# Kernel tuning notes

Measured on AMD Instinct MI355X. Metric: run time of the kernel, lower is better.

## Reference

```python
import jax, jax.numpy as jnp
import numpy as np

EMBED_DIM = 1024
NUM_HEADS = 16
HEAD_DIM = EMBED_DIM // NUM_HEADS


def setup_inputs() -> dict:
    key = jax.random.key(0)
    ks = jax.random.split(key, 9)
    B, S, E = 2, 2048, EMBED_DIM
    scale = 1.0 / np.sqrt(E)
    inputs = jax.random.normal(ks[0], (B, S, E), dtype=jnp.float32)
    # torch nn.Linear params: weight [out,in], bias [out]
    Wq = jax.random.uniform(ks[1], (E, E), jnp.float32, -scale, scale)
    bq = jax.random.uniform(ks[2], (E,), jnp.float32, -scale, scale)
    Wk = jax.random.uniform(ks[3], (E, E), jnp.float32, -scale, scale)
    bk = jax.random.uniform(ks[4], (E,), jnp.float32, -scale, scale)
    Wv = jax.random.uniform(ks[5], (E, E), jnp.float32, -scale, scale)
    bv = jax.random.uniform(ks[6], (E,), jnp.float32, -scale, scale)
    Wo = jax.random.uniform(ks[7], (E, E), jnp.float32, -scale, scale)
    bo = jax.random.uniform(ks[8], (E,), jnp.float32, -scale, scale)
    return {"inputs": inputs, "Wq": Wq, "bq": bq, "Wk": Wk, "bk": bk,
            "Wv": Wv, "bv": bv, "Wo": Wo, "bo": bo}


def _split_heads(x, B, S):
    # [B,S,E] -> [B,H,S,Dh]
    return x.reshape(B, S, NUM_HEADS, HEAD_DIM).transpose(0, 2, 1, 3)


def reference(inputs, Wq, bq, Wk, bk, Wv, bv, Wo, bo):
    B, S, E = inputs.shape
    q = _split_heads(inputs @ Wq.T + bq, B, S)
    k = _split_heads(inputs @ Wk.T + bk, B, S)
    v = _split_heads(inputs @ Wv.T + bv, B, S)
    inv_sqrt_dk = 1.0 / jnp.sqrt(jnp.float32(HEAD_DIM))
    scores = jnp.einsum('bhqd,bhkd->bhqk', q, k) * inv_sqrt_dk
    weights = jax.nn.softmax(scores, axis=-1)
    attn = jnp.einsum('bhqk,bhkd->bhqd', weights, v)
    concat = attn.transpose(0, 2, 1, 3).reshape(B, S, E)
    return concat @ Wo.T + bo
```

## Files before the change

### kernel.cpp

```cpp
#include <hip/hip_runtime.h>
#include <hip/hip_bf16.h>
#include <stdint.h>


typedef short bf16x8 __attribute__((ext_vector_type(8)));
typedef float f32x4 __attribute__((ext_vector_type(4)));

__device__ __forceinline__ unsigned short f2b(float x) {
    unsigned b = __float_as_uint(x);
    b += 0x7FFFu + ((b >> 16) & 1u);
    return (unsigned short)(b >> 16);
}
__device__ __forceinline__ float b2f(unsigned short u) {
    return __uint_as_float(((unsigned)u) << 16);
}
__device__ __forceinline__ f32x4 mfma16(bf16x8 a, bf16x8 b, f32x4 c) {
    return __builtin_amdgcn_mfma_f32_16x16x32_bf16(a, b, c, 0, 0, 0);
}
__device__ __forceinline__ void gl16(const void* g, void* l) {
    __builtin_amdgcn_global_load_lds(
        (const __attribute__((address_space(1))) void*)g,
        (__attribute__((address_space(3))) void*)l, 16, 0, 0);
}

__global__ __launch_bounds__(256)
void round4_kernel(const float* __restrict__ X, const float* __restrict__ Wq,
                   const float* __restrict__ Wk, const float* __restrict__ Wv,
                   unsigned short* __restrict__ Xh, unsigned short* __restrict__ Wh) {
    int i = blockIdx.x * 256 + threadIdx.x;
    const float4* src;
    ushort4* dst;
    if (i < 1048576) {
        src = (const float4*)X + i;
        dst = (ushort4*)Xh + i;
    } else {
        const int j = i - 1048576;
        const int w = j >> 18;
        const int k = j & 262143;
        const float* S = (w == 0) ? Wq : (w == 1) ? Wk : Wv;
        src = (const float4*)S + k;
        dst = (ushort4*)Wh + j;
    }
    float4 v = *src;
    ushort4 h;
    h.x = f2b(v.x); h.y = f2b(v.y); h.z = f2b(v.z); h.w = f2b(v.w);
    *dst = h;
}

__global__ void split_kernel(const float* __restrict__ src,
                             unsigned short* __restrict__ hi,
                             unsigned short* __restrict__ lo, int n4) {
    int i = blockIdx.x * blockDim.x + threadIdx.x;
    if (i >= n4) return;
    float4 v = reinterpret_cast<const float4*>(src)[i];
    ushort4 h, l;
    h.x = f2b(v.x); l.x = f2b(v.x - b2f(h.x));
    h.y = f2b(v.y); l.y = f2b(v.y - b2f(h.y));
    h.z = f2b(v.z); l.z = f2b(v.z - b2f(h.z));
    h.w = f2b(v.w); l.w = f2b(v.w - b2f(h.w));
    reinterpret_cast<ushort4*>(hi)[i] = h;
    reinterpret_cast<ushort4*>(lo)[i] = l;
}

__global__ __launch_bounds__(256, 2)
void gemm_qkv(const unsigned short* __restrict__ Xh, const unsigned short* __restrict__ Wh,
              const float* __restrict__ bias,
              unsigned short* __restrict__ Qs,
              unsigned short* __restrict__ Kh,
              unsigned short* __restrict__ Vh) {
    __shared__ __align__(16) unsigned short sA[128][32];
    __shared__ __align__(16) unsigned short sB[128][32];

    const int tid = threadIdx.x;
    const int lane = tid & 63;
    const int wid = tid >> 6;
    const int wr = wid >> 1, wc = wid & 1;
    const int m0 = blockIdx.y * 128, n0 = blockIdx.x * 128;
    const int fr = lane & 15;
    const int fo = (lane >> 4) << 3;
    const int rgrp = lane >> 4;
    constexpr float SC = 0.18033688011112042f;

    f32x4 zero4 = {0.f, 0.f, 0.f, 0.f};
    f32x4 acc[4][4];
#pragma unroll
    for (int i = 0; i < 4; i++)
#pragma unroll
        for (int j = 0; j < 4; j++) acc[i][j] = zero4;

    for (int k0 = 0; k0 < 1024; k0 += 32) {
        __syncthreads();
#pragma unroll
        for (int q = 0; q < 2; q++) {
            const int u = q * 256 + tid;
            const int row = u >> 2, c = u & 3;
            gl16(Xh + (size_t)(m0 + row) * 1024 + k0 + c * 8, (char*)&sA[0][0] + u * 16);
            gl16(Wh + (size_t)(n0 + row) * 1024 + k0 + c * 8, (char*)&sB[0][0] + u * 16);
        }
        __syncthreads();

        bf16x8 aF[4], bF[4];
#pragma unroll
        for (int i = 0; i < 4; i++) {
            aF[i] = *(const bf16x8*)&sA[wr * 64 + i * 16 + fr][fo];
            bF[i] = *(const bf16x8*)&sB[wc * 64 + i * 16 + fr][fo];
        }
#pragma unroll
        for (int i = 0; i < 4; i++)
#pragma unroll
            for (int j = 0; j < 4; j++)
                acc[i][j] = mfma16(aF[i], bF[j], acc[i][j]);
    }

#pragma unroll
    for (int i = 0; i < 4; i++) {
#pragma unroll
        for (int j = 0; j < 4; j++) {
            const int col = n0 + wc * 64 + j * 16 + fr;
            const float bv = bias[col];
            const int which = col >> 10;
            const int nn = col & 1023;
            const int h = nn >> 6, d = nn & 63;
#pragma unroll
            for (int r = 0; r < 4; r++) {
                const int row = m0 + wr * 64 + i * 16 + rgrp * 4 + r;
                const float v = acc[i][j][r] + bv;
                const int b = row >> 11, s = row & 2047;
                const size_t o = (((size_t)(b * 16 + h)) * 2048 + s) * 64 + d;
                if (which == 0)      Qs[o] = f2b(v * SC);
                else if (which == 1) Kh[o] = f2b(v);
                else                 Vh[o] = f2b(v);
            }
        }
    }
}

__global__ __launch_bounds__(256)
void vtrans(const unsigned short* __restrict__ V, unsigned short* __restrict__ Vt) {
    __shared__ unsigned short L[64][72];
    const int t = threadIdx.x;
    const int bh = blockIdx.y, s0 = blockIdx.x * 64;
    const size_t ib = (size_t)bh * 2048 * 64;
    const int srow = t >> 2, sc = (t & 3) * 16;
    *(uint4*)&L[srow][sc]     = *(const uint4*)(V + ib + (size_t)(s0 + srow) * 64 + sc);
    *(uint4*)&L[srow][sc + 8] = *(const uint4*)(V + ib + (size_t)(s0 + srow) * 64 + sc + 8);
    __syncthreads();
    const int d = t >> 2, k0 = (t & 3) * 16;
    unsigned short tmp[16];
#pragma unroll
    for (int i = 0; i < 16; i++) tmp[i] = L[k0 + i][d];
    *(uint4*)(Vt + ib + (size_t)d * 2048 + s0 + k0)     = *(uint4*)&tmp[0];
    *(uint4*)(Vt + ib + (size_t)d * 2048 + s0 + k0 + 8) = *(uint4*)&tmp[8];
}

__global__ __launch_bounds__(512)
void attn_kernel(const unsigned short* __restrict__ Qs,
                 const unsigned short* __restrict__ Kh,
                 const unsigned short* __restrict__ Vt,
                 unsigned short* __restrict__ OutHi, unsigned short* __restrict__ OutLo) {
    __shared__ __align__(16) unsigned short sK[2][64][64];
    __shared__ __align__(16) unsigned short sV[2][64][64];

    const int tid = threadIdx.x, lane = tid & 63, wid = tid >> 6;
    const int bh = blockIdx.y;
    const int q0 = blockIdx.x * 128;
    const int fr = lane & 15, fo = (lane >> 4) << 3, rgrp = lane >> 4;
    const size_t baseQK = (size_t)bh * 2048 * 64;
    const size_t baseVt = (size_t)bh * 64 * 2048;

    const int srow = tid >> 3, sc = tid & 7;
    const int klofs = srow * 128 + ((sc ^ (srow & 7)) << 4);
    const int cc0 = 4 * (sc >> 2) + 2 * (sc & 1);
    const int vbyte = 8 * ((sc >> 1) & 1);
    const int vlofs0 = srow * 128 + ((cc0 ^ (srow & 7)) << 4) + vbyte;
    const int vlofs1 = srow * 128 + (((cc0 + 1) ^ (srow & 7)) << 4) + vbyte;

    bf16x8 qh[2];
    {
        const size_t qoff = baseQK + (size_t)(q0 + wid * 16 + fr) * 64;
        qh[0] = *(const bf16x8*)(Qs + qoff + fo);
        qh[1] = *(const bf16x8*)(Qs + qoff + 32 + fo);
    }

    f32x4 zero4 = {0.f, 0.f, 0.f, 0.f};
    f32x4 accO[4];
#pragma unroll
    for (int i = 0; i < 4; i++) accO[i] = zero4;
    float accLp = 0.f;

    auto ldsw = [&](const unsigned short* S, int row, int c) -> bf16x8 {
        return *(const bf16x8*)((const char*)S + row * 128 + ((c ^ (row & 7)) << 4));
    };

    uint4 kreg, vreg;
    kreg = *(const uint4*)(Kh + baseQK + (size_t)srow * 64 + sc * 8);
    vreg = *(const uint4*)(Vt + baseVt + (size_t)srow * 2048 + sc * 8);
    *(uint4*)((char*)&sK[0][0][0] + klofs) = kreg;
    *(uint2*)((char*)&sV[0][0][0] + vlofs0) = make_uint2(vreg.x, vreg.y);
    *(uint2*)((char*)&sV[0][0][0] + vlofs1) = make_uint2(vreg.z, vreg.w);
    __syncthreads();

    int cur = 0;
    for (int kt = 0; kt < 2048; kt += 64) {
        const bool more = (kt + 64) < 2048;
        if (more) {
            kreg = *(const uint4*)(Kh + baseQK + (size_t)(kt + 64 + srow) * 64 + sc * 8);
            vreg = *(const uint4*)(Vt + baseVt + (size_t)srow * 2048 + kt + 64 + sc * 8);
        }

        const unsigned short* sKc = &sK[cur][0][0];
        const unsigned short* sVc = &sV[cur][0][0];

        f32x4 s4[4];
        __builtin_amdgcn_s_setprio(1);
#pragma unroll
        for (int nf = 0; nf < 4; nf++) {
            const int kr_ = nf * 16 + fr;
            f32x4 sa = mfma16(ldsw(sKc, kr_, rgrp), qh[0], zero4);
            sa = mfma16(ldsw(sKc, kr_, 4 + rgrp), qh[1], sa);
            s4[nf] = sa;
        }
        __builtin_amdgcn_s_setprio(0);

        float psum = 0.f;
        unsigned w[8];
#pragma unroll
        for (int nf = 0; nf < 4; nf++) {
            const float p0 = exp2f(s4[nf][0]);
            const float p1 = exp2f(s4[nf][1]);
            const float p2 = exp2f(s4[nf][2]);
            const float p3 = exp2f(s4[nf][3]);
            psum += (p0 + p1) + (p2 + p3);
            asm("v_cvt_pk_bf16_f32 %0, %1, %2" : "=v"(w[nf * 2])     : "v"(p0), "v"(p1));
            asm("v_cvt_pk_bf16_f32 %0, %1, %2" : "=v"(w[nf * 2 + 1]) : "v"(p2), "v"(p3));
        }
        accLp += psum;

        uint4 pw0 = {w[0], w[1], w[2], w[3]};
        uint4 pw1 = {w[4], w[5], w[6], w[7]};
        bf16x8 pf0 = *reinterpret_cast<bf16x8*>(&pw0);
        bf16x8 pf1 = *reinterpret_cast<bf16x8*>(&pw1);

        __builtin_amdgcn_s_setprio(1);
#pragma unroll
        for (int df = 0; df < 4; df++) {
            const int vrw = df * 16 + fr;
            f32x4 a = accO[df];
            a = mfma16(ldsw(sVc, vrw, rgrp), pf0, a);
            a = mfma16(ldsw(sVc, vrw, 4 + rgrp), pf1, a);
            accO[df] = a;
        }
        __builtin_amdgcn_s_setprio(0);

        if (more) {
            char* kb = (char*)&sK[cur ^ 1][0][0];
            char* vb = (char*)&sV[cur ^ 1][0][0];
            *(uint4*)(kb + klofs) = kreg;
            *(uint2*)(vb + vlofs0) = make_uint2(vreg.x, vreg.y);
            *(uint2*)(vb + vlofs1) = make_uint2(vreg.z, vreg.w);
        }
        __syncthreads();
        cur ^= 1;
    }

    float accL = accLp;
    accL += __shfl_xor(accL, 16);
    accL += __shfl_xor(accL, 32);

    const int b = bh >> 4, h = bh & 15;
    const int s = q0 + wid * 16 + fr;
    const float rL = 1.0f / accL;
#pragma unroll
    for (int df = 0; df < 4; df++) {
#pragma unroll
        for (int r = 0; r < 4; r++) {
            const int d = df * 16 + rgrp * 4 + r;
            const float v = accO[df][r] * rL;
            const size_t o = ((size_t)(b * 2048 + s)) * 1024 + h * 64 + d;
            const unsigned short hv = f2b(v);
            OutHi[o] = hv;
            OutLo[o] = f2b(v - b2f(hv));
        }
    }
}

__global__ __launch_bounds__(256, 2)
void gemm_out(const unsigned short* __restrict__ Ahi, const unsigned short* __restrict__ Alo,
              const unsigned short* __restrict__ Bhi, const unsigned short* __restrict__ Blo,
              const float* __restrict__ bias, float* __restrict__ outF) {
    __shared__ __align__(16) unsigned short sAh[128][32];
    __shared__ __align__(16) unsigned short sAl[128][32];
    __shared__ __align__(16) unsigned short sBh[128][32];
    __shared__ __align__(16) unsigned short sBl[128][32];

    const int tid = threadIdx.x;
    const int lane = tid & 63;
    const int wid = tid >> 6;
    const int wr = wid >> 1, wc = wid & 1;
    const int m0 = blockIdx.y * 128, n0 = blockIdx.x * 128;
    const int fr = lane & 15;
    const int fo = (lane >> 4) << 3;
    const int rgrp = lane >> 4;

    f32x4 zero4 = {0.f, 0.f, 0.f, 0.f};
    f32x4 acc[4][4];
#pragma unroll
    for (int i = 0; i < 4; i++)
#pragma unroll
        for (int j = 0; j < 4; j++) acc[i][j] = zero4;

    for (int k0 = 0; k0 < 1024; k0 += 32) {
        __syncthreads();
#pragma unroll
        for (int q = 0; q < 2; q++) {
            const int u = (wid * 2 + q) * 64 + lane;
            const int row = u >> 2, cs = u & 3;
            const size_t ga = (size_t)(m0 + row) * 1024 + k0 + cs * 8;
            const size_t gb = (size_t)(n0 + row) * 1024 + k0 + cs * 8;
            gl16(Ahi + ga, (char*)&sAh[0][0] + u * 16);
            gl16(Alo + ga, (char*)&sAl[0][0] + u * 16);
            gl16(Bhi + gb, (char*)&sBh[0][0] + u * 16);
            gl16(Blo + gb, (char*)&sBl[0][0] + u * 16);
        }
        __syncthreads();

        bf16x8 aH[4], aL[4], bH[4], bL[4];
#pragma unroll
        for (int i = 0; i < 4; i++) {
            aH[i] = *(const bf16x8*)&sAh[wr * 64 + i * 16 + fr][fo];
            aL[i] = *(const bf16x8*)&sAl[wr * 64 + i * 16 + fr][fo];
            bH[i] = *(const bf16x8*)&sBh[wc * 64 + i * 16 + fr][fo];
            bL[i] = *(const bf16x8*)&sBl[wc * 64 + i * 16 + fr][fo];
        }
#pragma unroll
        for (int i = 0; i < 4; i++)
#pragma unroll
            for (int j = 0; j < 4; j++) {
                acc[i][j] = mfma16(aH[i], bH[j], acc[i][j]);
                acc[i][j] = mfma16(aH[i], bL[j], acc[i][j]);
                acc[i][j] = mfma16(aL[i], bH[j], acc[i][j]);
            }
    }

#pragma unroll
    for (int i = 0; i < 4; i++) {
#pragma unroll
        for (int j = 0; j < 4; j++) {
            const int col = n0 + wc * 64 + j * 16 + fr;
            const float bv = bias[col];
#pragma unroll
            for (int r = 0; r < 4; r++) {
                const int row = m0 + wr * 64 + i * 16 + rgrp * 4 + r;
                outF[(size_t)row * 1024 + col] = acc[i][j][r] + bv;
            }
        }
    }
}

extern "C" void kernel_launch(void* const* d_in, const int* in_sizes, int n_in,
                              void* d_out, int out_size, void* d_ws, size_t ws_size,
                              hipStream_t stream) {
    const float* X  = (const float*)d_in[0];
    const float* Wq = (const float*)d_in[1];
    const float* bq = (const float*)d_in[2];
    const float* Wk = (const float*)d_in[3];
    const float* bk = (const float*)d_in[4];
    const float* Wv = (const float*)d_in[5];
    const float* bv = (const float*)d_in[6];
    const float* Wo = (const float*)d_in[7];
    const float* bo = (const float*)d_in[8];
    float* out = (float*)d_out;

    char* ws = (char*)d_ws;
    size_t off = 0;
    auto alloc = [&](size_t bytes) -> char* {
        char* p = ws + off;
        off += (bytes + 255) & ~(size_t)255;
        return p;
    };
    const size_t ME = (size_t)4096 * 1024;
    unsigned short* Xh     = (unsigned short*)alloc(ME * 2);
    unsigned short* Wqkvh  = (unsigned short*)alloc((size_t)3072 * 1024 * 2);
    unsigned short* Woh    = (unsigned short*)alloc((size_t)1024 * 1024 * 2);
    unsigned short* Wol    = (unsigned short*)alloc((size_t)1024 * 1024 * 2);
    float*          bqkv   = (float*)alloc(3072 * 4);
    unsigned short* Qsc    = (unsigned short*)alloc(ME * 2);
    unsigned short* Khb    = (unsigned short*)alloc(ME * 2);
    unsigned short* Vhb    = (unsigned short*)alloc(ME * 2);
    unsigned short* Vtb    = (unsigned short*)alloc(ME * 2);
    unsigned short* ATh    = (unsigned short*)alloc(ME * 2);
    unsigned short* ATl    = (unsigned short*)alloc(ME * 2);

    round4_kernel<<<7168, 256, 0, stream>>>(X, Wq, Wk, Wv, Xh, Wqkvh);
    split_kernel<<<1024, 256, 0, stream>>>(Wo, Woh, Wol, 262144);
    hipMemcpyAsync(bqkv,        bq, 4096, hipMemcpyDeviceToDevice, stream);
    hipMemcpyAsync(bqkv + 1024, bk, 4096, hipMemcpyDeviceToDevice, stream);
    hipMemcpyAsync(bqkv + 2048, bv, 4096, hipMemcpyDeviceToDevice, stream);

    gemm_qkv<<<dim3(24, 32), 256, 0, stream>>>(Xh, Wqkvh, bqkv, Qsc, Khb, Vhb);

    vtrans<<<dim3(32, 32), 256, 0, stream>>>(Vhb, Vtb);

    attn_kernel<<<dim3(16, 32), 512, 0, stream>>>(Qsc, Khb, Vtb, ATh, ATl);

    gemm_out<<<dim3(8, 32), 256, 0, stream>>>(ATh, ATl, Woh, Wol, bo, out);
}
```

Before: 243.8 us.

## Fuse prep kernels, remap attention blocks, and halve out-GEMM N tile

Merges the bf16 rounding kernel and the Wo hi/lo split kernel into one launch, which removes one kernel launch. Remaps attention block indices so that consecutive blocks fall on different heads, with the aim of spreading work across XCDs and their L2 caches. Halves the output GEMM N tile to 64, doubling the grid from 256 to 512 blocks so the GPU's compute units are better filled, at the cost of more A-tile reloads.

```diff
diff --git a/kernel.cpp b/kernel.cpp
--- a/kernel.cpp
+++ b/kernel.cpp
@@ -24,42 +24,41 @@
 }
 
 __global__ __launch_bounds__(256)
-void round4_kernel(const float* __restrict__ X, const float* __restrict__ Wq,
-                   const float* __restrict__ Wk, const float* __restrict__ Wv,
-                   unsigned short* __restrict__ Xh, unsigned short* __restrict__ Wh) {
+void prep_kernel(const float* __restrict__ X, const float* __restrict__ Wq,
+                 const float* __restrict__ Wk, const float* __restrict__ Wv,
+                 const float* __restrict__ Wo,
+                 unsigned short* __restrict__ Xh, unsigned short* __restrict__ Wh,
+                 unsigned short* __restrict__ Woh, unsigned short* __restrict__ Wol) {
     int i = blockIdx.x * 256 + threadIdx.x;
-    const float4* src;
-    ushort4* dst;
-    if (i < 1048576) {
-        src = (const float4*)X + i;
-        dst = (ushort4*)Xh + i;
+    if (i < 1835008) {
+        const float4* src;
+        ushort4* dst;
+        if (i < 1048576) {
+            src = (const float4*)X + i;
+            dst = (ushort4*)Xh + i;
+        } else {
+            const int j = i - 1048576;
+            const int w = j >> 18;
+            const int k = j & 262143;
+            const float* S = (w == 0) ? Wq : (w == 1) ? Wk : Wv;
+            src = (const float4*)S + k;
+            dst = (ushort4*)Wh + j;
+        }
+        float4 v = *src;
+        ushort4 h;
+        h.x = f2b(v.x); h.y = f2b(v.y); h.z = f2b(v.z); h.w = f2b(v.w);
+        *dst = h;
     } else {
-        const int j = i - 1048576;
-        const int w = j >> 18;
-        const int k = j & 262143;
-        const float* S = (w == 0) ? Wq : (w == 1) ? Wk : Wv;
-        src = (const float4*)S + k;
-        dst = (ushort4*)Wh + j;
-    }
-    float4 v = *src;
-    ushort4 h;
-    h.x = f2b(v.x); h.y = f2b(v.y); h.z = f2b(v.z); h.w = f2b(v.w);
-    *dst = h;
-}
-
-__global__ void split_kernel(const float* __restrict__ src,
-                             unsigned short* __restrict__ hi,
-                             unsigned short* __restrict__ lo, int n4) {
-    int i = blockIdx.x * blockDim.x + threadIdx.x;
-    if (i >= n4) return;
-    float4 v = reinterpret_cast<const float4*>(src)[i];
-    ushort4 h, l;
-    h.x = f2b(v.x); l.x = f2b(v.x - b2f(h.x));
-    h.y = f2b(v.y); l.y = f2b(v.y - b2f(h.y));
-    h.z = f2b(v.z); l.z = f2b(v.z - b2f(h.z));
-    h.w = f2b(v.w); l.w = f2b(v.w - b2f(h.w));
-    reinterpret_cast<ushort4*>(hi)[i] = h;
-    reinterpret_cast<ushort4*>(lo)[i] = l;
+        const int j = i - 1835008;
+        float4 v = reinterpret_cast<const float4*>(Wo)[j];
+        ushort4 h, l;
+        h.x = f2b(v.x); l.x = f2b(v.x - b2f(h.x));
+        h.y = f2b(v.y); l.y = f2b(v.y - b2f(h.y));
+        h.z = f2b(v.z); l.z = f2b(v.z - b2f(h.z));
+        h.w = f2b(v.w); l.w = f2b(v.w - b2f(h.w));
+        reinterpret_cast<ushort4*>(Woh)[j] = h;
+        reinterpret_cast<ushort4*>(Wol)[j] = l;
+    }
 }
 
 __global__ __launch_bounds__(256, 2)
@@ -162,8 +161,9 @@
     __shared__ __align__(16) unsigned short sV[2][64][64];
 
     const int tid = threadIdx.x, lane = tid & 63, wid = tid >> 6;
-    const int bh = blockIdx.y;
-    const int q0 = blockIdx.x * 128;
+    const int flat = blockIdx.x + (blockIdx.y << 4);
+    const int bh = (flat & 7) * 4 + (flat >> 7);
+    const int q0 = ((flat >> 3) & 15) * 128;
     const int fr = lane & 15, fo = (lane >> 4) << 3, rgrp = lane >> 4;
     const size_t baseQK = (size_t)bh * 2048 * 64;
     const size_t baseVt = (size_t)bh * 64 * 2048;
@@ -290,52 +290,58 @@
               const float* __restrict__ bias, float* __restrict__ outF) {
     __shared__ __align__(16) unsigned short sAh[128][32];
     __shared__ __align__(16) unsigned short sAl[128][32];
-    __shared__ __align__(16) unsigned short sBh[128][32];
-    __shared__ __align__(16) unsigned short sBl[128][32];
+    __shared__ __align__(16) unsigned short sBh[64][32];
+    __shared__ __align__(16) unsigned short sBl[64][32];
 
     const int tid = threadIdx.x;
     const int lane = tid & 63;
     const int wid = tid >> 6;
     const int wr = wid >> 1, wc = wid & 1;
-    const int m0 = blockIdx.y * 128, n0 = blockIdx.x * 128;
+    const int m0 = blockIdx.y * 128, n0 = blockIdx.x * 64;
     const int fr = lane & 15;
     const int fo = (lane >> 4) << 3;
     const int rgrp = lane >> 4;
 
     f32x4 zero4 = {0.f, 0.f, 0.f, 0.f};
-    f32x4 acc[4][4];
+    f32x4 acc[4][2];
 #pragma unroll
     for (int i = 0; i < 4; i++)
 #pragma unroll
-        for (int j = 0; j < 4; j++) acc[i][j] = zero4;
+        for (int j = 0; j < 2; j++) acc[i][j] = zero4;
 
     for (int k0 = 0; k0 < 1024; k0 += 32) {
         __syncthreads();
 #pragma unroll
         for (int q = 0; q < 2; q++) {
-            const int u = (wid * 2 + q) * 64 + lane;
-            const int row = u >> 2, cs = u & 3;
-            const size_t ga = (size_t)(m0 + row) * 1024 + k0 + cs * 8;
-            const size_t gb = (size_t)(n0 + row) * 1024 + k0 + cs * 8;
+            const int u = q * 256 + tid;
+            const int row = u >> 2, c = u & 3;
+            const size_t ga = (size_t)(m0 + row) * 1024 + k0 + c * 8;
             gl16(Ahi + ga, (char*)&sAh[0][0] + u * 16);
             gl16(Alo + ga, (char*)&sAl[0][0] + u * 16);
-            gl16(Bhi + gb, (char*)&sBh[0][0] + u * 16);
-            gl16(Blo + gb, (char*)&sBl[0][0] + u * 16);
+        }
+        {
+            const int row = tid >> 2, c = tid & 3;
+            const size_t gb = (size_t)(n0 + row) * 1024 + k0 + c * 8;
+            gl16(Bhi + gb, (char*)&sBh[0][0] + tid * 16);
+            gl16(Blo + gb, (char*)&sBl[0][0] + tid * 16);
         }
         __syncthreads();
 
-        bf16x8 aH[4], aL[4], bH[4], bL[4];
+        bf16x8 aH[4], aL[4], bH[2], bL[2];
 #pragma unroll
         for (int i = 0; i < 4; i++) {
             aH[i] = *(const bf16x8*)&sAh[wr * 64 + i * 16 + fr][fo];
             aL[i] = *(const bf16x8*)&sAl[wr * 64 + i * 16 + fr][fo];
-            bH[i] = *(const bf16x8*)&sBh[wc * 64 + i * 16 + fr][fo];
-            bL[i] = *(const bf16x8*)&sBl[wc * 64 + i * 16 + fr][fo];
+        }
+#pragma unroll
+        for (int j = 0; j < 2; j++) {
+            bH[j] = *(const bf16x8*)&sBh[wc * 32 + j * 16 + fr][fo];
+            bL[j] = *(const bf16x8*)&sBl[wc * 32 + j * 16 + fr][fo];
         }
 #pragma unroll
         for (int i = 0; i < 4; i++)
 #pragma unroll
-            for (int j = 0; j < 4; j++) {
+            for (int j = 0; j < 2; j++) {
                 acc[i][j] = mfma16(aH[i], bH[j], acc[i][j]);
                 acc[i][j] = mfma16(aH[i], bL[j], acc[i][j]);
                 acc[i][j] = mfma16(aL[i], bH[j], acc[i][j]);
@@ -345,8 +351,8 @@
 #pragma unroll
     for (int i = 0; i < 4; i++) {
 #pragma unroll
-        for (int j = 0; j < 4; j++) {
-            const int col = n0 + wc * 64 + j * 16 + fr;
+        for (int j = 0; j < 2; j++) {
+            const int col = n0 + wc * 32 + j * 16 + fr;
             const float bv = bias[col];
 #pragma unroll
             for (int r = 0; r < 4; r++) {
@@ -391,8 +397,7 @@
     unsigned short* ATh    = (unsigned short*)alloc(ME * 2);
     unsigned short* ATl    = (unsigned short*)alloc(ME * 2);
 
-    round4_kernel<<<7168, 256, 0, stream>>>(X, Wq, Wk, Wv, Xh, Wqkvh);
-    split_kernel<<<1024, 256, 0, stream>>>(Wo, Woh, Wol, 262144);
+    prep_kernel<<<8192, 256, 0, stream>>>(X, Wq, Wk, Wv, Wo, Xh, Wqkvh, Woh, Wol);
     hipMemcpyAsync(bqkv,        bq, 4096, hipMemcpyDeviceToDevice, stream);
     hipMemcpyAsync(bqkv + 1024, bk, 4096, hipMemcpyDeviceToDevice, stream);
     hipMemcpyAsync(bqkv + 2048, bv, 4096, hipMemcpyDeviceToDevice, stream);
@@ -403,5 +408,5 @@
 
     attn_kernel<<<dim3(16, 32), 512, 0, stream>>>(Qsc, Khb, Vtb, ATh, ATl);
 
-    gemm_out<<<dim3(8, 32), 256, 0, stream>>>(ATh, ATl, Woh, Wol, bo, out);
-}
+    gemm_out<<<dim3(16, 32), 256, 0, stream>>>(ATh, ATl, Woh, Wol, bo, out);
+}
```

Result: faster. 233.3 us (-4.3%).
